# Kernel optimization log

Measured on AMD Instinct MI355X. Metric: run time of the kernel, lower is better.

The kernel has to match this reference:

```python
import jax, jax.numpy as jnp
import numpy as np

N, DV, M, DC = 1024, 4, 512, 8
E = N * DV  # 4096 edges; N*DV == M*DC
EPS32 = jnp.float32(1.1920929e-07)  # torch.finfo(torch.float32).eps


def _build_masks():
    rng = np.random.default_rng(0)
    var_of_edge = np.repeat(np.arange(N), DV)                # edge -> variable node
    chk_of_edge = rng.permutation(np.repeat(np.arange(M), DC))  # edge -> check node
    eye = np.eye(E, dtype=bool)
    w_in_to_odd = np.zeros((N, E), dtype=np.float32)
    w_in_to_odd[var_of_edge, np.arange(E)] = 1.0
    same_var = var_of_edge[:, None] == var_of_edge[None, :]
    same_chk = chk_of_edge[:, None] == chk_of_edge[None, :]
    w_even_to_odd = (same_var & ~eye).astype(np.float32)     # extrinsic var-node connectivity
    w_odd_to_even = (same_chk & ~eye).astype(np.float32)     # extrinsic check-node connectivity
    w_even_to_out = np.zeros((E, N), dtype=np.float32)
    w_even_to_out[np.arange(E), var_of_edge] = 1.0
    return w_in_to_odd, w_odd_to_even, w_even_to_odd, w_even_to_out


def setup_inputs() -> dict:
    key = jax.random.key(0)
    w_in_to_odd, w_odd_to_even, w_even_to_odd, w_even_to_out = _build_masks()
    x = 2.0 * jax.random.normal(key, (N, 1), dtype=jnp.float32)  # channel LLRs
    return {
        "x": x,
        "w_in_to_odd": jnp.asarray(w_in_to_odd),
        "w_odd_to_even": jnp.asarray(w_odd_to_even),
        "w_even_to_odd": jnp.asarray(w_even_to_odd),
        "w_even_to_out": jnp.asarray(w_even_to_out),
    }


def _activation_even(odd, w_odd_to_even):
    # odd: [E,1]; repeat across columns then mask -> aux[i,j] = w[i,j]*odd[i]
    aux = w_odd_to_even * odd                      # [E,E]
    aux = jnp.where(aux == 0.0, 1.0, aux)          # zeros (non-edges) -> multiplicative identity
    v = jnp.prod(aux, axis=0)                      # [E] product over incoming messages
    v = jnp.where(v >= 1.0, 1.0 - EPS32, v)
    v = jnp.where(v <= -1.0, -1.0 + EPS32, v)
    return (2.0 * jnp.arctanh(v))[:, None]         # [E,1]


def reference(x, w_in_to_odd, w_odd_to_even, w_even_to_odd, w_even_to_out):
    llr_part = w_in_to_odd.T @ x                   # [E,1], reused every odd layer
    # layer 1: even input is zeros (first_even_layer_output / first_w_even_to_odd)
    odd = jnp.tanh(0.5 * llr_part)
    even = _activation_even(odd, w_odd_to_even)
    for _ in range(4):                             # iterations 2..5 (shared 'rnn'/'spa' weights)
        odd = jnp.tanh(0.5 * (llr_part + w_even_to_odd.T @ even))
        even = _activation_even(odd, w_odd_to_even)
    out = x + w_even_to_out.T @ even               # [N,1]
    return jax.nn.sigmoid(out)
```

## Files before the change

### kernel.cpp

```cpp
#include <hip/hip_runtime.h>


#define En 4096
#define Nn 1024
#define Mn 512
#define EPSF 1.1920929e-07f

__global__ __launch_bounds__(256) void extract_checks(
    const float* __restrict__ w, int* __restrict__ counter,
    int* __restrict__ ce) {
  __shared__ int buf[4][8];
  const int lane = threadIdx.x & 63;
  const int wv   = threadIdx.x >> 6;
  const int row  = blockIdx.x * 4 + wv;
  const float4* rowp = (const float4*)(w + (size_t)row * En);

  int base = ((row + 1) >> 8) << 8;
  int cnt  = 0;
  for (; base < En; base += 256) {
    float4 v = rowp[(base >> 2) + lane];
    int col  = base + lane * 4;
#pragma unroll
    for (int k = 0; k < 4; ++k) {
      float val = (k == 0) ? v.x : (k == 1) ? v.y : (k == 2) ? v.z : v.w;
      bool hit  = (val != 0.0f) && (col + k > row);
      unsigned long long m = __ballot(hit);
      if (hit) {
        int idx = cnt + __popcll(m & ((1ull << lane) - 1ull));
        if (idx < 8) buf[wv][idx] = col + k;
      }
      cnt += __popcll(m);
    }
  }
  __syncthreads();
  if (cnt == 7 && lane == 0) {
    int slot = atomicAdd(counter, 1);
    int* dst = ce + slot * 8;
    dst[0] = row;
#pragma unroll
    for (int k = 0; k < 7; ++k) dst[k + 1] = buf[wv][k];
  }
}

__global__ __launch_bounds__(1024) void solve(
    const float* __restrict__ x, const int* __restrict__ ce_g,
    float* __restrict__ out) {
  __shared__ int   ce[Mn * 8];
  __shared__ float ods[En];
  __shared__ float evs[En];
  const int t = threadIdx.x;

#pragma unroll
  for (int k = 0; k < 4; ++k) ce[t + k * 1024] = ce_g[t + k * 1024];

  const float xt = x[t];
  const float th0 = tanhf(0.5f * xt);
#pragma unroll
  for (int k = 0; k < 4; ++k) ods[4 * t + k] = th0;
  __syncthreads();

  for (int it = 0; it < 5; ++it) {
    if (t < Mn) {
      int e[8];
      float f[8];
#pragma unroll
      for (int k = 0; k < 8; ++k) e[k] = ce[t * 8 + k];
#pragma unroll
      for (int k = 0; k < 8; ++k) {
        float o = ods[e[k]];
        f[k] = (o == 0.0f) ? 1.0f : o;
      }
#pragma unroll
      for (int k = 0; k < 8; ++k) {
        float v = 1.0f;
#pragma unroll
        for (int j = 0; j < 8; ++j)
          if (j != k) v *= f[j];
        if (v >= 1.0f)       v =  1.0f - EPSF;
        else if (v <= -1.0f) v = -1.0f + EPSF;
        evs[e[k]] = 2.0f * atanhf(v);
      }
    }
    __syncthreads();

    if (it < 4) {
      float ev[4];
#pragma unroll
      for (int k = 0; k < 4; ++k) ev[k] = evs[4 * t + k];
#pragma unroll
      for (int k = 0; k < 4; ++k) {
        float s = 0.0f;
#pragma unroll
        for (int j = 0; j < 4; ++j)
          if (j != k) s += ev[j];
        ods[4 * t + k] = tanhf(0.5f * (xt + s));
      }
      __syncthreads();
    }
  }

  float s4 = evs[4 * t] + evs[4 * t + 1] + evs[4 * t + 2] + evs[4 * t + 3];
  float z  = xt + s4;
  out[t]   = 1.0f / (1.0f + expf(-z));
}

extern "C" void kernel_launch(void* const* d_in, const int* in_sizes, int n_in,
                              void* d_out, int out_size, void* d_ws,
                              size_t ws_size, hipStream_t stream) {
  const float* x    = (const float*)d_in[0];
  const float* w_oe = (const float*)d_in[2];
  float* out = (float*)d_out;

  int* counter = (int*)d_ws;
  int* ce      = (int*)((char*)d_ws + 256);

  hipMemsetAsync(d_ws, 0, 256, stream);
  extract_checks<<<dim3(1024), dim3(256), 0, stream>>>(w_oe, counter, ce);
  solve<<<dim3(1), dim3(1024), 0, stream>>>(x, ce, out);
}
```

Before: 175.9 us.

## Find only first peer per row and rebuild check groups in solve kernel

The mask-scan kernel now stops at the first nonzero column of each row of w_odd_to_even instead of scanning the rest of the row to collect all seven peers. This roughly halves the average bytes read from the large dense matrix, and the memset and the global atomic slot counter are removed. The single-block solve kernel then rebuilds the check groups from these first-peer pointers using shared-memory atomics and an insertion sort. The cost is extra setup work and synchronisation inside the serial one-block kernel.

```diff
diff --git a/kernel.cpp b/kernel.cpp
--- a/kernel.cpp
+++ b/kernel.cpp
@@ -6,54 +6,78 @@
 #define Mn 512
 #define EPSF 1.1920929e-07f
 
-__global__ __launch_bounds__(256) void extract_checks(
-    const float* __restrict__ w, int* __restrict__ counter,
-    int* __restrict__ ce) {
-  __shared__ int buf[4][8];
+__global__ __launch_bounds__(256) void find_first_peer(
+    const float* __restrict__ w, int* __restrict__ f) {
   const int lane = threadIdx.x & 63;
   const int wv   = threadIdx.x >> 6;
   const int row  = blockIdx.x * 4 + wv;
   const float4* rowp = (const float4*)(w + (size_t)row * En);
 
-  int base = ((row + 1) >> 8) << 8;
-  int cnt  = 0;
-  for (; base < En; base += 256) {
+  for (int base = 0; base < En; base += 256) {
     float4 v = rowp[(base >> 2) + lane];
-    int col  = base + lane * 4;
-#pragma unroll
-    for (int k = 0; k < 4; ++k) {
-      float val = (k == 0) ? v.x : (k == 1) ? v.y : (k == 2) ? v.z : v.w;
-      bool hit  = (val != 0.0f) && (col + k > row);
-      unsigned long long m = __ballot(hit);
-      if (hit) {
-        int idx = cnt + __popcll(m & ((1ull << lane) - 1ull));
-        if (idx < 8) buf[wv][idx] = col + k;
+    bool any = (v.x != 0.0f) | (v.y != 0.0f) | (v.z != 0.0f) | (v.w != 0.0f);
+    unsigned long long m = __ballot(any);
+    if (m) {
+      if (lane == __ffsll((unsigned long long)m) - 1) {
+        int off = (v.x != 0.0f) ? 0 : (v.y != 0.0f) ? 1 : (v.z != 0.0f) ? 2 : 3;
+        f[row] = base + 4 * lane + off;
       }
-      cnt += __popcll(m);
+      break;
     }
-  }
-  __syncthreads();
-  if (cnt == 7 && lane == 0) {
-    int slot = atomicAdd(counter, 1);
-    int* dst = ce + slot * 8;
-    dst[0] = row;
-#pragma unroll
-    for (int k = 0; k < 7; ++k) dst[k + 1] = buf[wv][k];
   }
 }
 
 __global__ __launch_bounds__(1024) void solve(
-    const float* __restrict__ x, const int* __restrict__ ce_g,
+    const float* __restrict__ x, const int* __restrict__ f_g,
     float* __restrict__ out) {
-  __shared__ int   ce[Mn * 8];
+  __shared__ int   fs[En];
+  __shared__ int   slotmap[En];
+  __shared__ int   ce[En];
   __shared__ float ods[En];
   __shared__ float evs[En];
+  __shared__ int   cnt[Mn];
+  __shared__ int   nchk;
   const int t = threadIdx.x;
 
 #pragma unroll
-  for (int k = 0; k < 4; ++k) ce[t + k * 1024] = ce_g[t + k * 1024];
+  for (int k = 0; k < 4; ++k) fs[t + k * 1024] = f_g[t + k * 1024];
+  if (t < Mn) cnt[t] = 0;
+  if (t == 0) nchk = 0;
+  __syncthreads();
 
-  const float xt = x[t];
+  int keys[4];
+#pragma unroll
+  for (int k = 0; k < 4; ++k) {
+    int e   = 4 * t + k;
+    int fe  = fs[e];
+    int ffe = fs[fe];
+    int key = (ffe == e && e < fe) ? e : fe;
+    keys[k] = key;
+    if (key == e) slotmap[e] = atomicAdd(&nchk, 1);
+  }
+  __syncthreads();
+#pragma unroll
+  for (int k = 0; k < 4; ++k) {
+    int e = 4 * t + k;
+    int c = slotmap[keys[k]];
+    int p = atomicAdd(&cnt[c], 1);
+    ce[c * 8 + p] = e;
+  }
+  __syncthreads();
+  if (t < Mn) {
+    int v[8];
+#pragma unroll
+    for (int k = 0; k < 8; ++k) v[k] = ce[t * 8 + k];
+    for (int i = 1; i < 8; ++i) {
+      int key = v[i], j = i - 1;
+      for (; j >= 0 && v[j] > key; --j) v[j + 1] = v[j];
+      v[j + 1] = key;
+    }
+#pragma unroll
+    for (int k = 0; k < 8; ++k) ce[t * 8 + k] = v[k];
+  }
+
+  const float xt  = x[t];
   const float th0 = tanhf(0.5f * xt);
 #pragma unroll
   for (int k = 0; k < 4; ++k) ods[4 * t + k] = th0;
@@ -111,10 +135,8 @@
   const float* w_oe = (const float*)d_in[2];
   float* out = (float*)d_out;
 
-  int* counter = (int*)d_ws;
-  int* ce      = (int*)((char*)d_ws + 256);
+  int* f = (int*)d_ws;
 
-  hipMemsetAsync(d_ws, 0, 256, stream);
-  extract_checks<<<dim3(1024), dim3(256), 0, stream>>>(w_oe, counter, ce);
-  solve<<<dim3(1), dim3(1024), 0, stream>>>(x, ce, out);
+  find_first_peer<<<dim3(1024), dim3(256), 0, stream>>>(w_oe, f);
+  solve<<<dim3(1), dim3(1024), 0, stream>>>(x, f, out);
 }
```

Result: faster. 171.1 us (-2.7%).
